# Performance work log

Hardware: AMD Instinct MI355X
Metric: run time of the kernel (lower is better)

## Reference

```python
import jax, jax.numpy as jnp
import numpy as np

D, H, HKV, HD = 1024, 16, 4, 64
ROPE_BASE = 10000.0
QK_GAIN_INIT = 1.0


def setup_inputs() -> dict:
    key = jax.random.key(0)
    ks = jax.random.split(key, 6)
    B, S = 2, 2048
    kv_dim = HKV * HD
    x = jax.random.normal(ks[0], (B, S, D), dtype=jnp.float32)
    Wq = jax.random.normal(ks[1], (D, D), dtype=jnp.float32) * 0.02
    Wk = jax.random.normal(ks[2], (kv_dim, D), dtype=jnp.float32) * 0.02
    Wv = jax.random.normal(ks[3], (kv_dim, D), dtype=jnp.float32) * 0.02
    Wo = jax.random.normal(ks[4], (D, D), dtype=jnp.float32) * 0.02
    q_gain = jnp.full((H,), QK_GAIN_INIT, dtype=jnp.float32)
    return {"x": x, "Wq": Wq, "Wk": Wk, "Wv": Wv, "Wo": Wo, "q_gain": q_gain}


def _rms_norm(t):
    eps = jnp.finfo(t.dtype).eps
    return t * jax.lax.rsqrt(jnp.mean(t * t, axis=-1, keepdims=True) + eps)


def _rope(t, cos, sin):
    # t: [B,h,S,HD]; cos/sin: [1,1,S,HD//2]
    half = t.shape[-1] // 2
    t1, t2 = t[..., :half], t[..., half:]
    return jnp.concatenate((t1 * cos + t2 * sin, -t1 * sin + t2 * cos), axis=-1)


def _attention(x, Wq, Wk, Wv, Wo, q_gain):
    B, S, _ = x.shape
    q = (x @ Wq.T).reshape(B, S, H, HD).transpose(0, 2, 1, 3)     # [B,H,S,HD]
    k = (x @ Wk.T).reshape(B, S, HKV, HD).transpose(0, 2, 1, 3)   # [B,HKV,S,HD]
    v = (x @ Wv.T).reshape(B, S, HKV, HD).transpose(0, 2, 1, 3)
    q, k = _rms_norm(q), _rms_norm(k)
    # rotary tables
    inv_freq = 1.0 / (ROPE_BASE ** (jnp.arange(0, HD, 2, dtype=jnp.float32) / HD))
    freqs = jnp.arange(S, dtype=jnp.float32)[:, None] * inv_freq[None, :]  # [S,HD//2]
    cos, sin = jnp.cos(freqs)[None, None], jnp.sin(freqs)[None, None]
    q, k = _rope(q, cos, sin), _rope(k, cos, sin)
    q = q * q_gain[None, :, None, None]
    # GQA: repeat kv heads to match query heads
    g = H // HKV
    k = jnp.repeat(k, g, axis=1)
    v = jnp.repeat(v, g, axis=1)
    scale = 1.0 / jnp.sqrt(jnp.asarray(HD, q.dtype))
    scores = jnp.einsum('bhqd,bhkd->bhqk', q, k) * scale
    causal = jnp.tril(jnp.ones((S, S), dtype=bool))
    scores = jnp.where(causal[None, None], scores, jnp.asarray(-jnp.inf, scores.dtype))
    attn = jax.nn.softmax(scores, axis=-1)
    y = jnp.einsum('bhqk,bhkd->bhqd', attn, v)                    # [B,H,S,HD]
    y = y.transpose(0, 2, 1, 3).reshape(B, S, D)
    return y @ Wo.T


def reference(x, Wq, Wk, Wv, Wo, q_gain):
    return _attention(x, Wq, Wk, Wv, Wo, q_gain)
```

## Files before the change

kernel.cpp:

```cpp
#include <hip/hip_runtime.h>
#include <hip/hip_bf16.h>
#include <math.h>

typedef __attribute__((ext_vector_type(8))) __bf16 bf16x8;
typedef __attribute__((ext_vector_type(4))) short short4v;
typedef __attribute__((ext_vector_type(4))) float f32x4;
typedef __attribute__((ext_vector_type(4))) unsigned short ushort4v;
typedef __attribute__((ext_vector_type(8))) unsigned short ushort8;

#define LOG2E 1.44269504088896340736f

static __device__ __forceinline__ unsigned short f2bf(float f) {
  unsigned int u = __float_as_uint(f);
  return (unsigned short)((u + 0x7fffu + ((u >> 16) & 1u)) >> 16);
}
static __device__ __forceinline__ short bfbits(float f) {
  __bf16 h = (__bf16)f;
  return __builtin_bit_cast(short, h);
}

static __device__ __forceinline__ void gload16(const unsigned short* g, void* l) {
  __builtin_amdgcn_global_load_lds(
      (const __attribute__((address_space(1))) unsigned int*)g,
      (__attribute__((address_space(3))) unsigned int*)l, 16, 0, 0);
}

__global__ __launch_bounds__(256) void prep_kernel(
    const float* __restrict__ x, const float* __restrict__ Wq,
    const float* __restrict__ Wk, const float* __restrict__ Wv,
    const float* __restrict__ Wo,
    unsigned short* __restrict__ xb, unsigned short* __restrict__ wqkv,
    unsigned short* __restrict__ wo_b, float* __restrict__ tab) {
  const int bx = blockIdx.x, tid = threadIdx.x;
  if (bx < 6656) {
    const float* src;
    unsigned short* dst;
    int i;
    if (bx < 4096)       { src = x;  dst = xb;             i = bx * 256 + tid; }
    else if (bx < 5120)  { src = Wq; dst = wqkv;           i = (bx - 4096) * 256 + tid; }
    else if (bx < 5376)  { src = Wk; dst = wqkv + 1048576; i = (bx - 5120) * 256 + tid; }
    else if (bx < 5632)  { src = Wv; dst = wqkv + 1310720; i = (bx - 5376) * 256 + tid; }
    else                 { src = Wo; dst = wo_b;           i = (bx - 5632) * 256 + tid; }
    float4 v = reinterpret_cast<const float4*>(src)[i];
    ushort4v o;
    o.x = f2bf(v.x); o.y = f2bf(v.y); o.z = f2bf(v.z); o.w = f2bf(v.w);
    reinterpret_cast<ushort4v*>(dst)[i] = o;
  } else {
    int i = (bx - 6656) * 256 + tid;
    int s = i >> 5, d = i & 31;
    float invf = powf(10000.f, -(float)d / 32.f);
    float fr = (float)s * invf;
    tab[s * 64 + d] = cosf(fr);
    tab[s * 64 + 32 + d] = sinf(fr);
  }
}

__global__ __launch_bounds__(256) void gemm_qkv_kernel(
    const unsigned short* __restrict__ A, const unsigned short* __restrict__ B,
    const float* __restrict__ tab, const float* __restrict__ qg,
    unsigned short* __restrict__ qb, unsigned short* __restrict__ kb,
    unsigned short* __restrict__ vtb) {
  __shared__ unsigned short sAll[64 * 64 + 128 * 64];
  unsigned short* sA = sAll;
  unsigned short* sB = sAll + 64 * 64;
  const int t = threadIdx.x;
  const int lane = t & 63;
  const int w = t >> 6;
  const int bm = blockIdx.x / 12, bn = blockIdx.x % 12;
  const long m0 = (long)bm * 64, n0 = (long)bn * 128;
  const int wm = (w >> 1) * 32, wn = (w & 1) * 64;
  const int lr = lane & 15, lg = lane >> 4;
  f32x4 acc[2][4];
#pragma unroll
  for (int i = 0; i < 2; i++)
#pragma unroll
    for (int j = 0; j < 4; j++) acc[i][j] = (f32x4){0.f, 0.f, 0.f, 0.f};

  for (int k0 = 0; k0 < 1024; k0 += 64) {
#pragma unroll
    for (int i = 0; i < 2; i++) {
      int chunk = i * 256 + t;
      int r = chunk >> 3;
      int c = (chunk & 7) << 3;
      gload16(A + (m0 + r) * 1024 + k0 + c, (char*)sA + chunk * 16);
    }
#pragma unroll
    for (int i = 0; i < 4; i++) {
      int chunk = i * 256 + t;
      int r = chunk >> 3;
      int c = (chunk & 7) << 3;
      gload16(B + (n0 + r) * 1024 + k0 + c, (char*)sB + chunk * 16);
    }
    __syncthreads();
#pragma unroll
    for (int kk = 0; kk < 2; ++kk) {
      bf16x8 af[2], bfr[4];
#pragma unroll
      for (int m = 0; m < 2; m++)
        af[m] = *(const bf16x8*)&sA[(wm + m * 16 + lr) * 64 + kk * 32 + lg * 8];
#pragma unroll
      for (int n = 0; n < 4; n++)
        bfr[n] = *(const bf16x8*)&sB[(wn + n * 16 + lr) * 64 + kk * 32 + lg * 8];
#pragma unroll
      for (int m = 0; m < 2; m++)
#pragma unroll
        for (int n = 0; n < 4; n++)
          acc[m][n] = __builtin_amdgcn_mfma_f32_16x16x32_bf16(af[m], bfr[n], acc[m][n], 0, 0, 0);
    }
    __syncthreads();
  }
  const int bb = (int)(m0 >> 11);
  const int s_base = (int)(m0 & 2047) + wm + lg * 4;
  const int hsel = wn >> 6;
  if (bn < 10) {
    float gscale = 1.0f;
    unsigned short* dstb;
    if (bn < 8) {
      gscale = qg[2 * bn + hsel] * (0.125f * LOG2E);
      dstb = qb + (size_t)(bb * 16 + 2 * bn + hsel) * 2048 * 64;
    } else {
      dstb = kb + (size_t)(bb * 4 + 2 * (bn - 8) + hsel) * 2048 * 64;
    }
#pragma unroll
    for (int m = 0; m < 2; m++) {
#pragma unroll
      for (int j = 0; j < 4; j++) {
        float ss = acc[m][0][j] * acc[m][0][j] + acc[m][1][j] * acc[m][1][j] +
                   acc[m][2][j] * acc[m][2][j] + acc[m][3][j] * acc[m][3][j];
        ss += __shfl_xor(ss, 1);
        ss += __shfl_xor(ss, 2);
        ss += __shfl_xor(ss, 4);
        ss += __shfl_xor(ss, 8);
        const float rinv = rsqrtf(ss * (1.0f / 64.0f) + 1.1920929e-07f);
        const int s = s_base + m * 16 + j;
        const float* tr = tab + s * 64;
        const float c0 = tr[lr], c1 = tr[16 + lr];
        const float s0 = tr[32 + lr], s1 = tr[48 + lr];
        const float n0v = acc[m][0][j] * rinv, n1v = acc[m][1][j] * rinv;
        const float n2v = acc[m][2][j] * rinv, n3v = acc[m][3][j] * rinv;
        float o0 = (n0v * c0 + n2v * s0) * gscale;
        float o1 = (n1v * c1 + n3v * s1) * gscale;
        float o2 = (n2v * c0 - n0v * s0) * gscale;
        float o3 = (n3v * c1 - n1v * s1) * gscale;
        unsigned short* d = dstb + (size_t)s * 64;
        d[lr]      = f2bf(o0);
        d[16 + lr] = f2bf(o1);
        d[32 + lr] = f2bf(o2);
        d[48 + lr] = f2bf(o3);
      }
    }
  } else {
    unsigned short* sT = sAll;
#pragma unroll
    for (int m = 0; m < 2; m++)
#pragma unroll
      for (int j = 0; j < 4; j++) {
        const int srow = wm + m * 16 + lg * 4 + j;
#pragma unroll
        for (int n = 0; n < 4; n++)
          sT[(hsel * 64 + srow) * 72 + n * 16 + lr] = f2bf(acc[m][n][j]);
      }
    __syncthreads();
    const int hd = t >> 7;
    const int d  = (t >> 1) & 63;
    const int sh = t & 1;
    const int hk = 2 * (bn - 10) + hd;
    unsigned short* dst = vtb + ((size_t)((bb * 4 + hk) * 64 + d)) * 2048 +
                          (int)(m0 & 2047) + sh * 32;
    ushort8 o;
#pragma unroll
    for (int c = 0; c < 4; ++c) {
#pragma unroll
      for (int k = 0; k < 8; ++k) o[k] = sT[(hd * 64 + sh * 32 + c * 8 + k) * 72 + d];
      *(ushort8*)(dst + c * 8) = o;
    }
  }
}

__global__ __launch_bounds__(256) void gemm_bt_kernel(
    const unsigned short* __restrict__ A, const unsigned short* __restrict__ B,
    float* __restrict__ C, int M, int N, int K, int nbn) {
  __shared__ unsigned short sA[64 * 64];
  __shared__ unsigned short sB[128 * 64];
  const int t = threadIdx.x;
  const int lane = t & 63;
  const int w = t >> 6;
  const int bm = blockIdx.x / nbn, bn = blockIdx.x % nbn;
  const long m0 = (long)bm * 64, n0 = (long)bn * 128;
  const int wm = (w >> 1) * 32, wn = (w & 1) * 64;
  const int lr = lane & 15, lg = lane >> 4;
  f32x4 acc[2][4];
#pragma unroll
  for (int i = 0; i < 2; i++)
#pragma unroll
    for (int j = 0; j < 4; j++) acc[i][j] = (f32x4){0.f, 0.f, 0.f, 0.f};

  for (int k0 = 0; k0 < K; k0 += 64) {
#pragma unroll
    for (int i = 0; i < 2; i++) {
      int chunk = i * 256 + t;
      int r = chunk >> 3;
      int c = (chunk & 7) << 3;
      gload16(A + (m0 + r) * (long)K + k0 + c, (char*)sA + chunk * 16);
    }
#pragma unroll
    for (int i = 0; i < 4; i++) {
      int chunk = i * 256 + t;
      int r = chunk >> 3;
      int c = (chunk & 7) << 3;
      gload16(B + (n0 + r) * (long)K + k0 + c, (char*)sB + chunk * 16);
    }
    __syncthreads();
#pragma unroll
    for (int kk = 0; kk < 2; ++kk) {
      bf16x8 af[2], bfr[4];
#pragma unroll
      for (int m = 0; m < 2; m++)
        af[m] = *(const bf16x8*)&sA[(wm + m * 16 + lr) * 64 + kk * 32 + lg * 8];
#pragma unroll
      for (int n = 0; n < 4; n++)
        bfr[n] = *(const bf16x8*)&sB[(wn + n * 16 + lr) * 64 + kk * 32 + lg * 8];
#pragma unroll
      for (int m = 0; m < 2; m++)
#pragma unroll
        for (int n = 0; n < 4; n++)
          acc[m][n] = __builtin_amdgcn_mfma_f32_16x16x32_bf16(af[m], bfr[n], acc[m][n], 0, 0, 0);
    }
    __syncthreads();
  }
#pragma unroll
  for (int m = 0; m < 2; m++) {
#pragma unroll
    for (int n = 0; n < 4; n++) {
      long col = n0 + wn + n * 16 + lr;
#pragma unroll
      for (int j = 0; j < 4; j++) {
        long row = m0 + wm + m * 16 + lg * 4 + j;
        C[row * N + col] = acc[m][n][j];
      }
    }
  }
}

__global__ __launch_bounds__(256) void attn_kernel(
    const unsigned short* __restrict__ qb, const unsigned short* __restrict__ kb,
    const unsigned short* __restrict__ vtb, unsigned short* __restrict__ yb,
    const float* __restrict__ qg) {
  __shared__ unsigned short sK[2][64 * 64];
  __shared__ unsigned short sV[2][64 * 64];
  const int tid = threadIdx.x;
  const int lane = tid & 63;
  const int w = tid >> 6;
  const int qt = 31 - (blockIdx.x >> 5);
  const int bh = blockIdx.x & 31;
  const int h = bh & 15;
  const int b = bh >> 4;
  const float M = 11.7f * fabsf(qg[h]);
  const int q0 = qt * 64 + w * 16;
  const unsigned short* Q  = qb  + (size_t)(b * 16 + h) * 2048 * 64;
  const unsigned short* Kp = kb  + (size_t)(b * 4 + (h >> 2)) * 2048 * 64;
  const unsigned short* Vp = vtb + (size_t)(b * 4 + (h >> 2)) * 64 * 2048;
  const int qc = lane & 15;
  const int g = lane >> 4;
  const int qrow = q0 + qc;
  const bf16x8 qf0 = *(const bf16x8*)(Q + (size_t)qrow * 64 + g * 8);
  const bf16x8 qf1 = *(const bf16x8*)(Q + (size_t)qrow * 64 + 32 + g * 8);
  f32x4 acc[4];
  acc[0] = acc[1] = acc[2] = acc[3] = (f32x4){0.f, 0.f, 0.f, 0.f};
  float lsum = 0.f;
  const int nt = qt + 1;

  const int r0 = tid >> 3, c0 = tid & 7;
  const int swz = ((c0 ^ (r0 & 7)) << 3);
  const unsigned short* gK = Kp + (size_t)r0 * 64 + swz;
  const unsigned short* gV = Vp + (size_t)r0 * 2048 + swz;

  gload16(gK,             (char*)&sK[0][0] + tid * 16);
  gload16(gK + 32 * 64,   (char*)&sK[0][0] + (tid + 256) * 16);
  gload16(gV,             (char*)&sV[0][0] + tid * 16);
  gload16(gV + 32 * 2048, (char*)&sV[0][0] + (tid + 256) * 16);
  gK += 64 * 64; gV += 64;

  int cur = 0;
  for (int t = 0; t < nt; ++t) {
    __syncthreads();
    if (t + 1 < nt) {
      const int nb = cur ^ 1;
      gload16(gK,             (char*)&sK[nb][0] + tid * 16);
      gload16(gK + 32 * 64,   (char*)&sK[nb][0] + (tid + 256) * 16);
      gload16(gV,             (char*)&sV[nb][0] + tid * 16);
      gload16(gV + 32 * 2048, (char*)&sV[nb][0] + (tid + 256) * 16);
      gK += 64 * 64; gV += 64;
    }
    const unsigned short* sKc = &sK[cur][0];
    const unsigned short* sVc = &sV[cur][0];
    f32x4 st[4];
    __builtin_amdgcn_s_setprio(1);
#pragma unroll
    for (int ks = 0; ks < 4; ++ks) {
      const int rr = ks * 16 + qc;
      bf16x8 kf0 = *(const bf16x8*)&sKc[rr * 64 + ((g ^ (rr & 7)) << 3)];
      bf16x8 kf1 = *(const bf16x8*)&sKc[rr * 64 + (((4 + g) ^ (rr & 7)) << 3)];
      f32x4 a = (f32x4){0.f, 0.f, 0.f, 0.f};
      a = __builtin_amdgcn_mfma_f32_16x16x32_bf16(kf0, qf0, a, 0, 0, 0);
      a = __builtin_amdgcn_mfma_f32_16x16x32_bf16(kf1, qf1, a, 0, 0, 0);
      st[ks] = a;
    }
    __builtin_amdgcn_s_setprio(0);
    if (t == nt - 1) {
#pragma unroll
      for (int ks = 0; ks < 4; ++ks)
#pragma unroll
        for (int j = 0; j < 4; ++j)
          if (ks * 16 + g * 4 + j > w * 16 + qc) st[ks][j] = -1e30f;
    }
    short4v pb[4];
#pragma unroll
    for (int ks = 0; ks < 4; ++ks)
#pragma unroll
      for (int j = 0; j < 4; ++j) {
        float p = exp2f(st[ks][j] - M);
        lsum += p;
        pb[ks][j] = bfbits(p);
      }
    __builtin_amdgcn_s_setprio(1);
#pragma unroll
    for (int ks = 0; ks < 4; ++ks) {
#pragma unroll
      for (int d = 0; d < 4; ++d) {
        const int rd = d * 16 + qc;
        const int el = rd * 64 + ((((ks * 2 + (g >> 1)) ^ (rd & 7)) << 3) + ((g & 1) << 2));
        short4v vf = *(const short4v*)&sVc[el];
        acc[d] = __builtin_amdgcn_mfma_f32_16x16x16bf16_1k(vf, pb[ks], acc[d], 0, 0, 0);
      }
    }
    __builtin_amdgcn_s_setprio(0);
    cur ^= 1;
  }
  float l = lsum;
  l += __shfl_xor(l, 16);
  l += __shfl_xor(l, 32);
  const float inv = 1.0f / l;
  unsigned short* Y = yb + (size_t)(b * 2048 + qrow) * 1024 + h * 64;
#pragma unroll
  for (int d = 0; d < 4; ++d) {
    ushort4v o;
#pragma unroll
    for (int j = 0; j < 4; ++j) o[j] = (unsigned short)bfbits(acc[d][j] * inv);
    *(ushort4v*)(Y + d * 16 + g * 4) = o;
  }
}

extern "C" void kernel_launch(void* const* d_in, const int* in_sizes, int n_in,
                              void* d_out, int out_size, void* d_ws, size_t ws_size,
                              hipStream_t stream) {
  const float* x  = (const float*)d_in[0];
  const float* Wq = (const float*)d_in[1];
  const float* Wk = (const float*)d_in[2];
  const float* Wv = (const float*)d_in[3];
  const float* Wo = (const float*)d_in[4];
  const float* qg = (const float*)d_in[5];
  float* out = (float*)d_out;

  char* ws = (char*)d_ws;
  const size_t NEED = 35127296;
  if (ws_size < NEED) return;
  unsigned short* xb   = (unsigned short*)(ws);
  unsigned short* wqkv = (unsigned short*)(ws + 8388608);
  unsigned short* wo_b = (unsigned short*)(ws + 11534336);
  unsigned short* qbuf = (unsigned short*)(ws + 13631488);
  unsigned short* kbuf = (unsigned short*)(ws + 22020096);
  unsigned short* vtb  = (unsigned short*)(ws + 24117248);
  unsigned short* ybuf = (unsigned short*)(ws + 26214400);
  float*          tab  = (float*)        (ws + 34603008);

  prep_kernel<<<6912, 256, 0, stream>>>(x, Wq, Wk, Wv, Wo, xb, wqkv, wo_b, tab);
  gemm_qkv_kernel<<<64 * 12, 256, 0, stream>>>(xb, wqkv, tab, qg, qbuf, kbuf, vtb);
  attn_kernel<<<1024, 256, 0, stream>>>(qbuf, kbuf, vtb, ybuf, qg);
  gemm_bt_kernel<<<64 * 8, 256, 0, stream>>>(ybuf, wo_b, out, 4096, 1024, 1024, 8);
}
```

Baseline: 105.3 us.

## Fuse fp32-to-bf16 conversion of x into QKV GEMM tile loads

The separate pass that converted x to bf16 in the prep kernel is removed. The QKV GEMM now reads fp32 x directly, converts it in registers and stores bf16 into shared memory, which drops a full write and read of the 16 MB activation buffer. The cost is that the A-tile loads become synchronous register loads rather than async global-to-LDS loads, and each of the 12 column blocks re-reads fp32 x at twice the bytes. Separately, the attention kernel precomputes its swizzled LDS byte offsets for K and V once instead of recomputing them every tile.

```diff
diff --git a/kernel.cpp b/kernel.cpp
--- a/kernel.cpp
+++ b/kernel.cpp
@@ -26,27 +26,25 @@
 }
 
 __global__ __launch_bounds__(256) void prep_kernel(
-    const float* __restrict__ x, const float* __restrict__ Wq,
-    const float* __restrict__ Wk, const float* __restrict__ Wv,
-    const float* __restrict__ Wo,
-    unsigned short* __restrict__ xb, unsigned short* __restrict__ wqkv,
-    unsigned short* __restrict__ wo_b, float* __restrict__ tab) {
+    const float* __restrict__ Wq, const float* __restrict__ Wk,
+    const float* __restrict__ Wv, const float* __restrict__ Wo,
+    unsigned short* __restrict__ wqkv, unsigned short* __restrict__ wo_b,
+    float* __restrict__ tab) {
   const int bx = blockIdx.x, tid = threadIdx.x;
-  if (bx < 6656) {
+  if (bx < 2560) {
     const float* src;
     unsigned short* dst;
     int i;
-    if (bx < 4096)       { src = x;  dst = xb;             i = bx * 256 + tid; }
-    else if (bx < 5120)  { src = Wq; dst = wqkv;           i = (bx - 4096) * 256 + tid; }
-    else if (bx < 5376)  { src = Wk; dst = wqkv + 1048576; i = (bx - 5120) * 256 + tid; }
-    else if (bx < 5632)  { src = Wv; dst = wqkv + 1310720; i = (bx - 5376) * 256 + tid; }
-    else                 { src = Wo; dst = wo_b;           i = (bx - 5632) * 256 + tid; }
+    if (bx < 1024)       { src = Wq; dst = wqkv;           i = bx * 256 + tid; }
+    else if (bx < 1280)  { src = Wk; dst = wqkv + 1048576; i = (bx - 1024) * 256 + tid; }
+    else if (bx < 1536)  { src = Wv; dst = wqkv + 1310720; i = (bx - 1280) * 256 + tid; }
+    else                 { src = Wo; dst = wo_b;           i = (bx - 1536) * 256 + tid; }
     float4 v = reinterpret_cast<const float4*>(src)[i];
     ushort4v o;
     o.x = f2bf(v.x); o.y = f2bf(v.y); o.z = f2bf(v.z); o.w = f2bf(v.w);
     reinterpret_cast<ushort4v*>(dst)[i] = o;
   } else {
-    int i = (bx - 6656) * 256 + tid;
+    int i = (bx - 2560) * 256 + tid;
     int s = i >> 5, d = i & 31;
     float invf = powf(10000.f, -(float)d / 32.f);
     float fr = (float)s * invf;
@@ -56,7 +54,7 @@
 }
 
 __global__ __launch_bounds__(256) void gemm_qkv_kernel(
-    const unsigned short* __restrict__ A, const unsigned short* __restrict__ B,
+    const float* __restrict__ X, const unsigned short* __restrict__ Bw,
     const float* __restrict__ tab, const float* __restrict__ qg,
     unsigned short* __restrict__ qb, unsigned short* __restrict__ kb,
     unsigned short* __restrict__ vtb) {
@@ -76,20 +74,28 @@
 #pragma unroll
     for (int j = 0; j < 4; j++) acc[i][j] = (f32x4){0.f, 0.f, 0.f, 0.f};
 
+  const int ar = t >> 3, ac = (t & 7) << 3;
   for (int k0 = 0; k0 < 1024; k0 += 64) {
-#pragma unroll
-    for (int i = 0; i < 2; i++) {
-      int chunk = i * 256 + t;
-      int r = chunk >> 3;
-      int c = (chunk & 7) << 3;
-      gload16(A + (m0 + r) * 1024 + k0 + c, (char*)sA + chunk * 16);
-    }
 #pragma unroll
     for (int i = 0; i < 4; i++) {
       int chunk = i * 256 + t;
       int r = chunk >> 3;
       int c = (chunk & 7) << 3;
-      gload16(B + (n0 + r) * 1024 + k0 + c, (char*)sB + chunk * 16);
+      gload16(Bw + (n0 + r) * 1024 + k0 + c, (char*)sB + chunk * 16);
+    }
+#pragma unroll
+    for (int i = 0; i < 2; i++) {
+      const int chunk = i * 256 + t;
+      const int r = ar + i * 32;
+      const float* src = X + (m0 + r) * 1024 + k0 + ac;
+      float4 f0 = *(const float4*)src;
+      float4 f1 = *(const float4*)(src + 4);
+      ushort8 u;
+      u[0] = (unsigned short)bfbits(f0.x); u[1] = (unsigned short)bfbits(f0.y);
+      u[2] = (unsigned short)bfbits(f0.z); u[3] = (unsigned short)bfbits(f0.w);
+      u[4] = (unsigned short)bfbits(f1.x); u[5] = (unsigned short)bfbits(f1.y);
+      u[6] = (unsigned short)bfbits(f1.z); u[7] = (unsigned short)bfbits(f1.w);
+      *(ushort8*)&sA[chunk * 8] = u;
     }
     __syncthreads();
 #pragma unroll
@@ -270,6 +276,21 @@
   float lsum = 0.f;
   const int nt = qt + 1;
 
+  int koff[4][2], voff[4][4];
+#pragma unroll
+  for (int ks = 0; ks < 4; ++ks) {
+    const int rr = ks * 16 + qc;
+    koff[ks][0] = (rr * 64 + ((g ^ (rr & 7)) << 3)) * 2;
+    koff[ks][1] = (rr * 64 + (((4 + g) ^ (rr & 7)) << 3)) * 2;
+  }
+#pragma unroll
+  for (int d = 0; d < 4; ++d) {
+    const int rd = d * 16 + qc;
+#pragma unroll
+    for (int ks = 0; ks < 4; ++ks)
+      voff[ks][d] = (rd * 64 + ((((ks * 2 + (g >> 1)) ^ (rd & 7)) << 3) + ((g & 1) << 2))) * 2;
+  }
+
   const int r0 = tid >> 3, c0 = tid & 7;
   const int swz = ((c0 ^ (r0 & 7)) << 3);
   const unsigned short* gK = Kp + (size_t)r0 * 64 + swz;
@@ -292,15 +313,14 @@
       gload16(gV + 32 * 2048, (char*)&sV[nb][0] + (tid + 256) * 16);
       gK += 64 * 64; gV += 64;
     }
-    const unsigned short* sKc = &sK[cur][0];
-    const unsigned short* sVc = &sV[cur][0];
+    const char* sKc = (const char*)&sK[cur][0];
+    const char* sVc = (const char*)&sV[cur][0];
     f32x4 st[4];
     __builtin_amdgcn_s_setprio(1);
 #pragma unroll
     for (int ks = 0; ks < 4; ++ks) {
-      const int rr = ks * 16 + qc;
-      bf16x8 kf0 = *(const bf16x8*)&sKc[rr * 64 + ((g ^ (rr & 7)) << 3)];
-      bf16x8 kf1 = *(const bf16x8*)&sKc[rr * 64 + (((4 + g) ^ (rr & 7)) << 3)];
+      bf16x8 kf0 = *(const bf16x8*)(sKc + koff[ks][0]);
+      bf16x8 kf1 = *(const bf16x8*)(sKc + koff[ks][1]);
       f32x4 a = (f32x4){0.f, 0.f, 0.f, 0.f};
       a = __builtin_amdgcn_mfma_f32_16x16x32_bf16(kf0, qf0, a, 0, 0, 0);
       a = __builtin_amdgcn_mfma_f32_16x16x32_bf16(kf1, qf1, a, 0, 0, 0);
@@ -328,9 +348,7 @@
     for (int ks = 0; ks < 4; ++ks) {
 #pragma unroll
       for (int d = 0; d < 4; ++d) {
-        const int rd = d * 16 + qc;
-        const int el = rd * 64 + ((((ks * 2 + (g >> 1)) ^ (rd & 7)) << 3) + ((g & 1) << 2));
-        short4v vf = *(const short4v*)&sVc[el];
+        short4v vf = *(const short4v*)(sVc + voff[ks][d]);
         acc[d] = __builtin_amdgcn_mfma_f32_16x16x16bf16_1k(vf, pb[ks], acc[d], 0, 0, 0);
       }
     }
@@ -363,19 +381,18 @@
   float* out = (float*)d_out;
 
   char* ws = (char*)d_ws;
-  const size_t NEED = 35127296;
+  const size_t NEED = 26738688;
   if (ws_size < NEED) return;
-  unsigned short* xb   = (unsigned short*)(ws);
-  unsigned short* wqkv = (unsigned short*)(ws + 8388608);
-  unsigned short* wo_b = (unsigned short*)(ws + 11534336);
-  unsigned short* qbuf = (unsigned short*)(ws + 13631488);
-  unsigned short* kbuf = (unsigned short*)(ws + 22020096);
-  unsigned short* vtb  = (unsigned short*)(ws + 24117248);
-  unsigned short* ybuf = (unsigned short*)(ws + 26214400);
-  float*          tab  = (float*)        (ws + 34603008);
-
-  prep_kernel<<<6912, 256, 0, stream>>>(x, Wq, Wk, Wv, Wo, xb, wqkv, wo_b, tab);
-  gemm_qkv_kernel<<<64 * 12, 256, 0, stream>>>(xb, wqkv, tab, qg, qbuf, kbuf, vtb);
+  unsigned short* wqkv = (unsigned short*)(ws);
+  unsigned short* wo_b = (unsigned short*)(ws + 3145728);
+  unsigned short* qbuf = (unsigned short*)(ws + 5242880);
+  unsigned short* kbuf = (unsigned short*)(ws + 13631488);
+  unsigned short* vtb  = (unsigned short*)(ws + 15728640);
+  unsigned short* ybuf = (unsigned short*)(ws + 17825792);
+  float*          tab  = (float*)        (ws + 26214400);
+
+  prep_kernel<<<2816, 256, 0, stream>>>(Wq, Wk, Wv, Wo, wqkv, wo_b, tab);
+  gemm_qkv_kernel<<<64 * 12, 256, 0, stream>>>(x, wqkv, tab, qg, qbuf, kbuf, vtb);
   attn_kernel<<<1024, 256, 0, stream>>>(qbuf, kbuf, vtb, ybuf, qg);
   gemm_bt_kernel<<<64 * 8, 256, 0, stream>>>(ybuf, wo_b, out, 4096, 1024, 1024, 8);
 }
```

New measurement: 107.4 us. +2.0%, slower.
